# Performance work log

Hardware: AMD Instinct MI355X
Metric: run time of the kernel (lower is better)

The kernel has to match this reference:

```python
import jax, jax.numpy as jnp
import numpy as np

N_NEURONS = 2048
IN_DIM = 1024
OUT_DIM = 1024
TOKENS = 4096
TIME_STEPS = 3
DENSITY = 0.25


def setup_inputs() -> dict:
    key = jax.random.key(0)
    ks = jax.random.split(key, 10)
    x = jax.random.normal(ks[0], (TOKENS, IN_DIM), dtype=jnp.float32)
    W_in = jax.random.normal(ks[1], (N_NEURONS, IN_DIM), dtype=jnp.float32) * (1.0 / np.sqrt(IN_DIM))
    b_in = jax.random.normal(ks[2], (N_NEURONS,), dtype=jnp.float32) * 0.01
    weights = jax.random.normal(ks[3], (N_NEURONS, N_NEURONS), dtype=jnp.float32) * 0.3
    J = jax.random.normal(ks[4], (N_NEURONS, N_NEURONS), dtype=jnp.float32) * 0.1
    theta = jax.random.uniform(ks[5], (N_NEURONS,), dtype=jnp.float32) * 1.0 + 0.25
    lam = jnp.asarray(0.35, dtype=jnp.float32)
    # connection mask: rand < density, zero diagonal (buffer, fixed)
    m = (jax.random.uniform(ks[6], (N_NEURONS, N_NEURONS)) < DENSITY).astype(jnp.float32)
    mask = m * (1.0 - jnp.eye(N_NEURONS, dtype=jnp.float32))
    noise_raw = jax.random.normal(ks[7], (TIME_STEPS, TOKENS, N_NEURONS), dtype=jnp.float32)
    W_out = jax.random.normal(ks[8], (OUT_DIM, N_NEURONS), dtype=jnp.float32) * (1.0 / np.sqrt(N_NEURONS))
    b_out = jax.random.normal(ks[9], (OUT_DIM,), dtype=jnp.float32) * 0.01
    return {"x": x, "W_in": W_in, "b_in": b_in, "weights": weights, "J": J,
            "theta": theta, "lam": lam, "mask": mask, "noise_raw": noise_raw,
            "W_out": W_out, "b_out": b_out, "time_steps": TIME_STEPS}


def reference(x, W_in, b_in, weights, J, theta, lam, mask, noise_raw, W_out, b_out, time_steps):
    # input projection: [tokens, in_dim] -> [tokens, n]
    state = x @ W_in.T + b_in
    eff_w = weights * mask          # [n, n]
    J_m = J * mask                  # [n, n]
    T = jnp.abs(jnp.sin(2.0 * theta))  # temperature [n]
    for t in range(time_steps):
        signal = state @ eff_w                     # [tokens, n]
        s = jnp.tanh(state)
        # einsum('bi,ij,bj->bj', s, J_m, s) == (s @ J_m) * s
        delta = (s @ J_m) * s                      # [tokens, n]
        noise = noise_raw[t] * T * 0.1             # [tokens, n]
        state = jnp.tanh(signal + lam * delta + noise)
    return state @ W_out.T + b_out
```

## Files before the change

kernel.cpp:

```cpp
#include <hip/hip_runtime.h>
#include <hip/hip_fp16.h>

#define TOKENS 4096
#define NN 2048
#define IN_DIM 1024
#define OUT_DIM 1024
#define TSTEPS 3

typedef _Float16 half8 __attribute__((ext_vector_type(8)));
typedef _Float16 half4 __attribute__((ext_vector_type(4)));
typedef float f32x4 __attribute__((ext_vector_type(4)));

__device__ __forceinline__ void gload_lds16(const void* g, void* l) {
    __builtin_amdgcn_global_load_lds(
        (const __attribute__((address_space(1))) unsigned*)g,
        (__attribute__((address_space(3))) unsigned*)l, 16, 0, 0);
}

__global__ __launch_bounds__(512, 2)
void dual_gemm(const _Float16* __restrict__ A0g, const _Float16* __restrict__ B0g,
               float* __restrict__ C0,
               const _Float16* __restrict__ A1g, const _Float16* __restrict__ B1g,
               float* __restrict__ C1)
{
    __shared__ __align__(16) _Float16 lds[2 * 32768];
    const int tid  = threadIdx.x;
    const int wid  = tid >> 6;
    const int lane = tid & 63;

    const int raw  = blockIdx.x;
    const int widx = (raw & 7) * 32 + (raw >> 3);
    const int g    = widx >> 7;
    const int bid  = widx & 127;
    const int by = bid >> 3;
    const int bx = bid & 7;
    const _Float16* __restrict__ A = g ? A1g : A0g;
    const _Float16* __restrict__ B = g ? B1g : B0g;
    float* __restrict__ C = g ? C1 : C0;
    const int brow = by << 8;
    const int bcol = bx << 8;

    const int sr = tid >> 3;
    const int sc = ((tid & 7) ^ (sr & 7)) << 3;
    const _Float16* gA = A + (size_t)(brow + sr) * NN + sc;
    const _Float16* gB = B + (size_t)(bcol + sr) * NN + sc;
    const int ldst = wid << 9;

    auto stA = [&](int T, int h) {
        _Float16* l = lds + (T & 1) * 32768 + h * 8192;
        const _Float16* p = gA + (size_t)(h << 7) * NN + (T << 6);
        gload_lds16(p,           l + ldst);
        gload_lds16(p + 64 * NN, l + 4096 + ldst);
    };
    auto stB = [&](int T, int h) {
        _Float16* l = lds + (T & 1) * 32768 + 16384 + h * 8192;
        const _Float16* p = gB + (size_t)(h << 7) * NN + (T << 6);
        gload_lds16(p,           l + ldst);
        gload_lds16(p + 64 * NN, l + 4096 + ldst);
    };

    const int wr = (wid >> 2) << 7;
    const int wc = (wid & 3) << 6;
    const int lr = lane & 15;
    const int lq = lane >> 4;
    const int x7 = lr & 7;
    const int c0 = (lq ^ x7) << 3;
    const int c1 = ((4 + lq) ^ x7) << 3;
    const int aRow = (wr + lr) << 6;
    const int bRow = 16384 + ((wc + lr) << 6);

    f32x4 acc[8][4];
#pragma unroll
    for (int m = 0; m < 8; ++m)
#pragma unroll
        for (int n = 0; n < 4; ++n) acc[m][n] = (f32x4){0.f, 0.f, 0.f, 0.f};

    half8 af[4][2], b0f[2][2], b1f[2][2];

    stA(0, 0); stA(0, 1); stB(0, 0); stB(0, 1);
    stA(1, 0); stA(1, 1); stB(1, 0); stB(1, 1);
    asm volatile("s_waitcnt vmcnt(8)" ::: "memory");
    __builtin_amdgcn_s_barrier();
    asm volatile("" ::: "memory");

    for (int T = 0; T < 32; ++T) {
        const _Float16* lb = lds + (T & 1) * 32768;

#pragma unroll
        for (int m = 0; m < 4; ++m) {
            af[m][0] = *(const half8*)&lb[aRow + (m << 10) + c0];
            af[m][1] = *(const half8*)&lb[aRow + (m << 10) + c1];
        }
#pragma unroll
        for (int n = 0; n < 2; ++n) {
            b0f[n][0] = *(const half8*)&lb[bRow + (n << 10) + c0];
            b0f[n][1] = *(const half8*)&lb[bRow + (n << 10) + c1];
        }
        __builtin_amdgcn_s_barrier();
        asm volatile("s_waitcnt lgkmcnt(0)" ::: "memory");
        __builtin_amdgcn_sched_barrier(0);
        __builtin_amdgcn_s_setprio(1);
#pragma unroll
        for (int kk = 0; kk < 2; ++kk)
#pragma unroll
            for (int m = 0; m < 4; ++m)
#pragma unroll
                for (int n = 0; n < 2; ++n)
                    acc[m][n] = __builtin_amdgcn_mfma_f32_16x16x32_f16(af[m][kk], b0f[n][kk], acc[m][n], 0, 0, 0);
        __builtin_amdgcn_s_setprio(0);
        __builtin_amdgcn_sched_barrier(0);
        __builtin_amdgcn_s_barrier();
        asm volatile("" ::: "memory");

#pragma unroll
        for (int n = 0; n < 2; ++n) {
            b1f[n][0] = *(const half8*)&lb[bRow + ((n + 2) << 10) + c0];
            b1f[n][1] = *(const half8*)&lb[bRow + ((n + 2) << 10) + c1];
        }
        __builtin_amdgcn_s_barrier();
        asm volatile("s_waitcnt lgkmcnt(0)" ::: "memory");
        __builtin_amdgcn_sched_barrier(0);
        __builtin_amdgcn_s_setprio(1);
#pragma unroll
        for (int kk = 0; kk < 2; ++kk)
#pragma unroll
            for (int m = 0; m < 4; ++m)
#pragma unroll
                for (int n = 0; n < 2; ++n)
                    acc[m][n + 2] = __builtin_amdgcn_mfma_f32_16x16x32_f16(af[m][kk], b1f[n][kk], acc[m][n + 2], 0, 0, 0);
        __builtin_amdgcn_s_setprio(0);
        __builtin_amdgcn_sched_barrier(0);
        __builtin_amdgcn_s_barrier();
        asm volatile("" ::: "memory");

#pragma unroll
        for (int m = 0; m < 4; ++m) {
            af[m][0] = *(const half8*)&lb[aRow + ((m + 4) << 10) + c0];
            af[m][1] = *(const half8*)&lb[aRow + ((m + 4) << 10) + c1];
        }
        if (T < 30) { stB(T + 2, 0); stB(T + 2, 1); }
        __builtin_amdgcn_s_barrier();
        asm volatile("s_waitcnt lgkmcnt(0)" ::: "memory");
        __builtin_amdgcn_sched_barrier(0);
        __builtin_amdgcn_s_setprio(1);
#pragma unroll
        for (int kk = 0; kk < 2; ++kk)
#pragma unroll
            for (int m = 0; m < 4; ++m)
#pragma unroll
                for (int n = 0; n < 2; ++n)
                    acc[m + 4][n] = __builtin_amdgcn_mfma_f32_16x16x32_f16(af[m][kk], b0f[n][kk], acc[m + 4][n], 0, 0, 0);
        __builtin_amdgcn_s_setprio(0);
        __builtin_amdgcn_sched_barrier(0);
        __builtin_amdgcn_s_barrier();
        asm volatile("" ::: "memory");

        if (T < 30) { stA(T + 2, 0); stA(T + 2, 1); }
        __builtin_amdgcn_s_setprio(1);
#pragma unroll
        for (int kk = 0; kk < 2; ++kk)
#pragma unroll
            for (int m = 0; m < 4; ++m)
#pragma unroll
                for (int n = 0; n < 2; ++n)
                    acc[m + 4][n + 2] = __builtin_amdgcn_mfma_f32_16x16x32_f16(af[m][kk], b1f[n][kk], acc[m + 4][n + 2], 0, 0, 0);
        __builtin_amdgcn_s_setprio(0);
        __builtin_amdgcn_sched_barrier(0);
        if (T < 30)       asm volatile("s_waitcnt vmcnt(8)" ::: "memory");
        else if (T == 30) asm volatile("s_waitcnt vmcnt(0)" ::: "memory");
        __builtin_amdgcn_s_barrier();
        asm volatile("" ::: "memory");
    }

    const int cr = lq << 2;
    const int cc = lane & 15;
#pragma unroll
    for (int m = 0; m < 8; ++m) {
#pragma unroll
        for (int n = 0; n < 4; ++n) {
            const size_t o0 = (size_t)(brow + wr + m * 16 + cr) * NN
                            + (bcol + wc + n * 16 + cc);
#pragma unroll
            for (int j = 0; j < 4; ++j)
                C[o0 + (size_t)j * NN] = acc[m][n][j];
        }
    }
}

template<int EPI>
__global__ __launch_bounds__(256)
void gemm_bt(const _Float16* __restrict__ A, const _Float16* __restrict__ B,
             float* __restrict__ C, const float* __restrict__ bias,
             _Float16* __restrict__ oSta, _Float16* __restrict__ oS,
             int M, int N, int K)
{
    __shared__ _Float16 As[128 * 32];
    __shared__ _Float16 Bs[128 * 32];
    const int tid  = threadIdx.x;
    const int wid  = tid >> 6;
    const int lane = tid & 63;
    const int wr = (wid >> 1) * 64;
    const int wc = (wid & 1) * 64;
    const int brow = blockIdx.y * 128;
    const int bcol = blockIdx.x * 128;

    f32x4 acc[4][4];
#pragma unroll
    for (int m = 0; m < 4; ++m)
#pragma unroll
        for (int n = 0; n < 4; ++n) acc[m][n] = (f32x4){0.f, 0.f, 0.f, 0.f};

    const int ldr = tid >> 2;
    const int ldc = (tid & 3) * 8;
    const int wbase = (wid << 4) * 32;
    const int kq = (lane >> 4) * 8;
    const int lr = lane & 15;

    for (int k0 = 0; k0 < K; k0 += 32) {
        __syncthreads();
        gload_lds16(A + (size_t)(brow + ldr) * K + k0 + ldc, As + wbase);
        gload_lds16(A + (size_t)(brow + 64 + ldr) * K + k0 + ldc, As + 64 * 32 + wbase);
        gload_lds16(B + (size_t)(bcol + ldr) * K + k0 + ldc, Bs + wbase);
        gload_lds16(B + (size_t)(bcol + 64 + ldr) * K + k0 + ldc, Bs + 64 * 32 + wbase);
        __syncthreads();

        half8 af[4], bf[4];
#pragma unroll
        for (int m = 0; m < 4; ++m)
            af[m] = *(const half8*)&As[(wr + m * 16 + lr) * 32 + kq];
#pragma unroll
        for (int n = 0; n < 4; ++n)
            bf[n] = *(const half8*)&Bs[(wc + n * 16 + lr) * 32 + kq];
#pragma unroll
        for (int m = 0; m < 4; ++m)
#pragma unroll
            for (int n = 0; n < 4; ++n)
                acc[m][n] = __builtin_amdgcn_mfma_f32_16x16x32_f16(af[m], bf[n], acc[m][n], 0, 0, 0);
    }

    const int cr = (lane >> 4) * 4;
    const int cc = lane & 15;
#pragma unroll
    for (int m = 0; m < 4; ++m) {
#pragma unroll
        for (int n = 0; n < 4; ++n) {
            const int ccol = bcol + wc + n * 16 + cc;
#pragma unroll
            for (int j = 0; j < 4; ++j) {
                const int crow = brow + wr + m * 16 + cr + j;
                float v = acc[m][n][j];
                const size_t o = (size_t)crow * N + ccol;
                if (EPI == 1) {
                    v += bias[ccol];
                    oSta[o] = (_Float16)v;
                    oS[o] = (_Float16)tanhf(v);
                } else {
                    C[o] = v + bias[ccol];
                }
            }
        }
    }
}

__global__ void cvt_f16(const float* __restrict__ in, _Float16* __restrict__ out, int n4) {
    int i = blockIdx.x * blockDim.x + threadIdx.x;
    if (i < n4) {
        f32x4 v = *(const f32x4*)&in[(size_t)i * 4];
        half4 h;
        h[0] = (_Float16)v[0]; h[1] = (_Float16)v[1];
        h[2] = (_Float16)v[2]; h[3] = (_Float16)v[3];
        *(half4*)&out[(size_t)i * 4] = h;
    }
}

__global__ void transmul2(const float* __restrict__ W, const float* __restrict__ J,
                          const float* __restrict__ Mk,
                          _Float16* __restrict__ effT, _Float16* __restrict__ JmT) {
    __shared__ float tw[32][33];
    __shared__ float tj[32][33];
    const int bx = blockIdx.x * 32, by = blockIdx.y * 32;
    const int tx = threadIdx.x, ty0 = threadIdx.y;
#pragma unroll
    for (int r = 0; r < 4; ++r) {
        int ty = ty0 + r * 8;
        size_t idx = (size_t)(by + ty) * NN + bx + tx;
        float mv = Mk[idx];
        tw[ty][tx] = W[idx] * mv;
        tj[ty][tx] = J[idx] * mv;
    }
    __syncthreads();
#pragma unroll
    for (int r = 0; r < 4; ++r) {
        int ty = ty0 + r * 8;
        size_t o = (size_t)(bx + ty) * NN + by + tx;
        effT[o] = (_Float16)tw[tx][ty];
        JmT[o]  = (_Float16)tj[tx][ty];
    }
}

__global__ void tsc_kernel(const float* __restrict__ theta, float* __restrict__ Tsc) {
    int i = blockIdx.x * blockDim.x + threadIdx.x;
    if (i < NN) Tsc[i] = fabsf(sinf(2.0f * theta[i])) * 0.1f;
}

__global__ void step_kernel(const float* __restrict__ signal, const float* __restrict__ sJ,
                            const float* __restrict__ noise, const float* __restrict__ Tsc,
                            const float* __restrict__ lamp,
                            _Float16* __restrict__ stateH, _Float16* __restrict__ sH) {
    const int i4 = blockIdx.x * blockDim.x + threadIdx.x;
    const float lam = lamp[0];
    const size_t base = (size_t)i4 * 4;
    f32x4 sg = *(const f32x4*)&signal[base];
    f32x4 dj = *(const f32x4*)&sJ[base];
    f32x4 nz = *(const f32x4*)&noise[base];
    const int col4 = (int)(base & (NN - 1));
    f32x4 tv = *(const f32x4*)&Tsc[col4];
    half4 so = *(const half4*)&sH[base];
    half4 hs, hn;
#pragma unroll
    for (int j = 0; j < 4; ++j) {
        float s = (float)so[j];
        float arg = sg[j] + lam * (dj[j] * s) + nz[j] * tv[j];
        float st = tanhf(arg);
        hs[j] = (_Float16)st;
        hn[j] = (_Float16)tanhf(st);
    }
    *(half4*)&stateH[base] = hs;
    *(half4*)&sH[base] = hn;
}

extern "C" void kernel_launch(void* const* d_in, const int* in_sizes, int n_in,
                              void* d_out, int out_size, void* d_ws, size_t ws_size,
                              hipStream_t stream) {
    const float* x       = (const float*)d_in[0];
    const float* W_in    = (const float*)d_in[1];
    const float* b_in    = (const float*)d_in[2];
    const float* weights = (const float*)d_in[3];
    const float* Jmat    = (const float*)d_in[4];
    const float* theta   = (const float*)d_in[5];
    const float* lam     = (const float*)d_in[6];
    const float* mask    = (const float*)d_in[7];
    const float* noise   = (const float*)d_in[8];
    const float* W_out   = (const float*)d_in[9];
    const float* b_out   = (const float*)d_in[10];
    float* out = (float*)d_out;

    char* w = (char*)d_ws;
    auto alloc = [&](size_t b) { char* p = w; w += (b + 255) & ~(size_t)255; return p; };
    _Float16* xh     = (_Float16*)alloc((size_t)TOKENS * IN_DIM * 2);
    _Float16* WinH   = (_Float16*)alloc((size_t)NN * IN_DIM * 2);
    _Float16* WoutH  = (_Float16*)alloc((size_t)OUT_DIM * NN * 2);
    _Float16* effT   = (_Float16*)alloc((size_t)NN * NN * 2);
    _Float16* JmT    = (_Float16*)alloc((size_t)NN * NN * 2);
    _Float16* stateH = (_Float16*)alloc((size_t)TOKENS * NN * 2);
    _Float16* sH     = (_Float16*)alloc((size_t)TOKENS * NN * 2);
    float* Tsc       = (float*)alloc((size_t)NN * 4);
    float* signal    = (float*)alloc((size_t)TOKENS * NN * 4);
    float* sJ        = (float*)alloc((size_t)TOKENS * NN * 4);

    cvt_f16<<<TOKENS * IN_DIM / 4 / 256, 256, 0, stream>>>(x, xh, TOKENS * IN_DIM / 4);
    cvt_f16<<<NN * IN_DIM / 4 / 256, 256, 0, stream>>>(W_in, WinH, NN * IN_DIM / 4);
    cvt_f16<<<OUT_DIM * NN / 4 / 256, 256, 0, stream>>>(W_out, WoutH, OUT_DIM * NN / 4);
    transmul2<<<dim3(NN / 32, NN / 32), dim3(32, 8), 0, stream>>>(weights, Jmat, mask, effT, JmT);
    tsc_kernel<<<NN / 256, 256, 0, stream>>>(theta, Tsc);

    gemm_bt<1><<<dim3(NN / 128, TOKENS / 128), 256, 0, stream>>>(
        xh, WinH, nullptr, b_in, stateH, sH, TOKENS, NN, IN_DIM);

    for (int t = 0; t < TSTEPS; ++t) {
        dual_gemm<<<256, 512, 0, stream>>>(stateH, effT, signal, sH, JmT, sJ);
        step_kernel<<<TOKENS * NN / 4 / 256, 256, 0, stream>>>(
            signal, sJ, noise + (size_t)t * TOKENS * NN, Tsc, lam, stateH, sH);
    }

    gemm_bt<2><<<dim3(OUT_DIM / 128, TOKENS / 128), 256, 0, stream>>>(
        stateH, WoutH, out, b_out, nullptr, nullptr, TOKENS, OUT_DIM, NN);
}
```

Baseline: 381.3 us.

## Restructure dual GEMM main loop to overlap LDS fragment reads with MFMA

Reorganizes the K-loop of the dual GEMM so the work is split along k-halves (c0/c1) instead of n-halves. Each LDS fragment load for the next MFMA group is issued before the current group runs, with partial lgkmcnt waits, and the first fragments of the next tile are prefetched right after the buffer-swap barrier. It also drops the per-phase barriers, leaving two per iteration, and issues all global-to-LDS copies for tile T+2 together. The intent is to hide LDS latency and cut synchronisation, at the cost of more live fragment registers under the 512x2 launch bound and a possible race if the waitcnt counts are wrong.

```diff
diff --git a/kernel.cpp b/kernel.cpp
--- a/kernel.cpp
+++ b/kernel.cpp
@@ -16,6 +16,10 @@
         (const __attribute__((address_space(1))) unsigned*)g,
         (__attribute__((address_space(3))) unsigned*)l, 16, 0, 0);
 }
+
+#define LGKM(N) asm volatile("s_waitcnt lgkmcnt(" #N ")" ::: "memory")
+#define VMCNT(N) asm volatile("s_waitcnt vmcnt(" #N ")" ::: "memory")
+#define SCHED0() __builtin_amdgcn_sched_barrier(0)
 
 __global__ __launch_bounds__(512, 2)
 void dual_gemm(const _Float16* __restrict__ A0g, const _Float16* __restrict__ B0g,
@@ -75,101 +79,88 @@
 #pragma unroll
         for (int n = 0; n < 4; ++n) acc[m][n] = (f32x4){0.f, 0.f, 0.f, 0.f};
 
-    half8 af[4][2], b0f[2][2], b1f[2][2];
+    half8 af0[4], af1[4], af2[4], af3[4], bf0[4], bf1[4];
 
     stA(0, 0); stA(0, 1); stB(0, 0); stB(0, 1);
     stA(1, 0); stA(1, 1); stB(1, 0); stB(1, 1);
-    asm volatile("s_waitcnt vmcnt(8)" ::: "memory");
+    VMCNT(8);
     __builtin_amdgcn_s_barrier();
-    asm volatile("" ::: "memory");
+    {
+        const _Float16* lb = lds;
+#pragma unroll
+        for (int m = 0; m < 4; ++m) af0[m] = *(const half8*)&lb[aRow + (m << 10) + c0];
+#pragma unroll
+        for (int n = 0; n < 4; ++n) bf0[n] = *(const half8*)&lb[bRow + (n << 10) + c0];
+    }
 
     for (int T = 0; T < 32; ++T) {
         const _Float16* lb = lds + (T & 1) * 32768;
 
 #pragma unroll
-        for (int m = 0; m < 4; ++m) {
-            af[m][0] = *(const half8*)&lb[aRow + (m << 10) + c0];
-            af[m][1] = *(const half8*)&lb[aRow + (m << 10) + c1];
-        }
-#pragma unroll
-        for (int n = 0; n < 2; ++n) {
-            b0f[n][0] = *(const half8*)&lb[bRow + (n << 10) + c0];
-            b0f[n][1] = *(const half8*)&lb[bRow + (n << 10) + c1];
-        }
+        for (int m = 0; m < 4; ++m) af1[m] = *(const half8*)&lb[aRow + ((m + 4) << 10) + c0];
+        LGKM(4);
+        SCHED0();
+        __builtin_amdgcn_s_setprio(1);
+#pragma unroll
+        for (int m = 0; m < 4; ++m)
+#pragma unroll
+            for (int n = 0; n < 4; ++n)
+                acc[m][n] = __builtin_amdgcn_mfma_f32_16x16x32_f16(af0[m], bf0[n], acc[m][n], 0, 0, 0);
+        __builtin_amdgcn_s_setprio(0);
+        SCHED0();
+
+#pragma unroll
+        for (int m = 0; m < 4; ++m) af2[m] = *(const half8*)&lb[aRow + (m << 10) + c1];
+#pragma unroll
+        for (int n = 0; n < 4; ++n) bf1[n] = *(const half8*)&lb[bRow + (n << 10) + c1];
+        LGKM(8);
+        SCHED0();
+        __builtin_amdgcn_s_setprio(1);
+#pragma unroll
+        for (int m = 0; m < 4; ++m)
+#pragma unroll
+            for (int n = 0; n < 4; ++n)
+                acc[m + 4][n] = __builtin_amdgcn_mfma_f32_16x16x32_f16(af1[m], bf0[n], acc[m + 4][n], 0, 0, 0);
+        __builtin_amdgcn_s_setprio(0);
+        SCHED0();
+
+#pragma unroll
+        for (int m = 0; m < 4; ++m) af3[m] = *(const half8*)&lb[aRow + ((m + 4) << 10) + c1];
+        LGKM(4);
+        SCHED0();
+        __builtin_amdgcn_s_setprio(1);
+#pragma unroll
+        for (int m = 0; m < 4; ++m)
+#pragma unroll
+            for (int n = 0; n < 4; ++n)
+                acc[m][n] = __builtin_amdgcn_mfma_f32_16x16x32_f16(af2[m], bf1[n], acc[m][n], 0, 0, 0);
+        __builtin_amdgcn_s_setprio(0);
+        SCHED0();
+
+        LGKM(0);
         __builtin_amdgcn_s_barrier();
-        asm volatile("s_waitcnt lgkmcnt(0)" ::: "memory");
-        __builtin_amdgcn_sched_barrier(0);
-        __builtin_amdgcn_s_setprio(1);
-#pragma unroll
-        for (int kk = 0; kk < 2; ++kk)
-#pragma unroll
-            for (int m = 0; m < 4; ++m)
-#pragma unroll
-                for (int n = 0; n < 2; ++n)
-                    acc[m][n] = __builtin_amdgcn_mfma_f32_16x16x32_f16(af[m][kk], b0f[n][kk], acc[m][n], 0, 0, 0);
-        __builtin_amdgcn_s_setprio(0);
-        __builtin_amdgcn_sched_barrier(0);
+        if (T < 30) { stA(T + 2, 0); stA(T + 2, 1); stB(T + 2, 0); stB(T + 2, 1); }
+        if (T < 30) { VMCNT(8); }
+        else        { VMCNT(0); }
         __builtin_amdgcn_s_barrier();
         asm volatile("" ::: "memory");
 
-#pragma unroll
-        for (int n = 0; n < 2; ++n) {
-            b1f[n][0] = *(const half8*)&lb[bRow + ((n + 2) << 10) + c0];
-            b1f[n][1] = *(const half8*)&lb[bRow + ((n + 2) << 10) + c1];
+        if (T < 31) {
+            const _Float16* ln = lds + ((T + 1) & 1) * 32768;
+#pragma unroll
+            for (int m = 0; m < 4; ++m) af0[m] = *(const half8*)&ln[aRow + (m << 10) + c0];
+#pragma unroll
+            for (int n = 0; n < 4; ++n) bf0[n] = *(const half8*)&ln[bRow + (n << 10) + c0];
         }
-        __builtin_amdgcn_s_barrier();
-        asm volatile("s_waitcnt lgkmcnt(0)" ::: "memory");
-        __builtin_amdgcn_sched_barrier(0);
+        SCHED0();
         __builtin_amdgcn_s_setprio(1);
 #pragma unroll
-        for (int kk = 0; kk < 2; ++kk)
-#pragma unroll
-            for (int m = 0; m < 4; ++m)
-#pragma unroll
-                for (int n = 0; n < 2; ++n)
-                    acc[m][n + 2] = __builtin_amdgcn_mfma_f32_16x16x32_f16(af[m][kk], b1f[n][kk], acc[m][n + 2], 0, 0, 0);
+        for (int m = 0; m < 4; ++m)
+#pragma unroll
+            for (int n = 0; n < 4; ++n)
+                acc[m + 4][n] = __builtin_amdgcn_mfma_f32_16x16x32_f16(af3[m], bf1[n], acc[m + 4][n], 0, 0, 0);
         __builtin_amdgcn_s_setprio(0);
-        __builtin_amdgcn_sched_barrier(0);
-        __builtin_amdgcn_s_barrier();
-        asm volatile("" ::: "memory");
-
-#pragma unroll
-        for (int m = 0; m < 4; ++m) {
-            af[m][0] = *(const half8*)&lb[aRow + ((m + 4) << 10) + c0];
-            af[m][1] = *(const half8*)&lb[aRow + ((m + 4) << 10) + c1];
-        }
-        if (T < 30) { stB(T + 2, 0); stB(T + 2, 1); }
-        __builtin_amdgcn_s_barrier();
-        asm volatile("s_waitcnt lgkmcnt(0)" ::: "memory");
-        __builtin_amdgcn_sched_barrier(0);
-        __builtin_amdgcn_s_setprio(1);
-#pragma unroll
-        for (int kk = 0; kk < 2; ++kk)
-#pragma unroll
-            for (int m = 0; m < 4; ++m)
-#pragma unroll
-                for (int n = 0; n < 2; ++n)
-                    acc[m + 4][n] = __builtin_amdgcn_mfma_f32_16x16x32_f16(af[m][kk], b0f[n][kk], acc[m + 4][n], 0, 0, 0);
-        __builtin_amdgcn_s_setprio(0);
-        __builtin_amdgcn_sched_barrier(0);
-        __builtin_amdgcn_s_barrier();
-        asm volatile("" ::: "memory");
-
-        if (T < 30) { stA(T + 2, 0); stA(T + 2, 1); }
-        __builtin_amdgcn_s_setprio(1);
-#pragma unroll
-        for (int kk = 0; kk < 2; ++kk)
-#pragma unroll
-            for (int m = 0; m < 4; ++m)
-#pragma unroll
-                for (int n = 0; n < 2; ++n)
-                    acc[m + 4][n + 2] = __builtin_amdgcn_mfma_f32_16x16x32_f16(af[m][kk], b1f[n][kk], acc[m + 4][n + 2], 0, 0, 0);
-        __builtin_amdgcn_s_setprio(0);
-        __builtin_amdgcn_sched_barrier(0);
-        if (T < 30)       asm volatile("s_waitcnt vmcnt(8)" ::: "memory");
-        else if (T == 30) asm volatile("s_waitcnt vmcnt(0)" ::: "memory");
-        __builtin_amdgcn_s_barrier();
-        asm volatile("" ::: "memory");
+        SCHED0();
     }
 
     const int cr = lq << 2;
```

Result: faster. 370.4 us (-2.9%).
